# Kernel optimization log

Hardware: AMD Instinct MI355X
Metric: run time of the kernel (lower is better)

The kernel has to match this reference:

```python
import jax, jax.numpy as jnp
import numpy as np

B, S, I, H, O, E, K = 2, 2048, 4096, 1376, 4096, 8, 2
BALANCE_W = 0.01  # balance_loss_weight in llama-moe


def setup_inputs() -> dict:
    key = jax.random.key(0)
    ks = jax.random.split(key, 6)
    sc = lambda k, shape, fan: jax.random.normal(k, shape, jnp.float32) * (fan ** -0.5)
    return {
        "x": jax.random.normal(ks[0], (B, S, I), jnp.float32),
        "gate_w": sc(ks[1], (E, I), I),          # linear gate network, no bias
        "w_gate": sc(ks[2], (E, H, I), I),       # GLU gate proj per expert
        "b_gate": jnp.zeros((E, H), jnp.float32),
        "w_up": sc(ks[3], (E, H, I), I),         # GLU up proj per expert
        "b_up": jnp.zeros((E, H), jnp.float32),
        "w_down": sc(ks[4], (E, O, H), H),       # down proj per expert
        "b_down": jnp.zeros((E, O), jnp.float32),
    }


def _cv_squared(v, eps=1e-10):
    # torch: x.var() / (x.mean()**2 + eps), unbiased variance
    mean = jnp.mean(v)
    var = jnp.sum((v - mean) ** 2) / (v.shape[0] - 1)
    return var / (mean ** 2 + eps)


def reference(x, gate_w, w_gate, b_gate, w_up, b_up, w_down, b_down):
    bsz, seq, _ = x.shape
    xt = x.reshape(-1, I)                         # [T, I] tokens
    T = xt.shape[0]

    # ---- TopKBalancedNoisyGate (no-noise branch) ----
    logits = xt @ gate_w.T                        # [T, E]
    top_logits, top_idx = jax.lax.top_k(logits, K)
    top_scores = jax.nn.softmax(top_logits, axis=-1)   # softmax over top-k logits
    # dense routing matrix: zeros.scatter(1, top_idx, top_scores)
    dense = jnp.zeros((T, E), xt.dtype).at[jnp.arange(T)[:, None], top_idx].set(top_scores)
    importance = dense.sum(axis=0)                # [E]
    load = (dense > 0).astype(jnp.float32).sum(axis=0)  # [E]
    gate_loss = BALANCE_W * (_cv_squared(importance) + _cv_squared(load))

    # ---- UniversalCalculator over LinearGLUExperts ----
    # Dense-dispatch formulation: compute every expert on every token, weight by
    # the (mostly-zero) routing matrix -> identical math to gather/grouped-GEMM/scatter.
    g = jnp.einsum('ti,ehi->teh', xt, w_gate) + b_gate        # [T, E, H]
    u = jnp.einsum('ti,ehi->teh', xt, w_up) + b_up            # [T, E, H]
    inter = jax.nn.silu(g) * u                                # GLU
    # score * (W_down h + b_down) == W_down (score*h) + score*b_down
    y = jnp.einsum('teh,eoh->to', inter * dense[:, :, None], w_down) + dense @ b_down
    return y.reshape(bsz, seq, O), gate_loss
```

## Files before the change

### kernel.cpp

```cpp
#include <hip/hip_runtime.h>
#include <hip/hip_bf16.h>
#include <stdint.h>

#define TN 4096
#define DI 4096
#define DH 1376
#define DHP 1408
#define DO 4096
#define NE 8
#define NPAIR 8192

typedef unsigned short u16;
typedef __bf16 bf16x8 __attribute__((ext_vector_type(8)));
typedef float f32x4 __attribute__((ext_vector_type(4)));
typedef uint32_t u32x4 __attribute__((ext_vector_type(4)));

__device__ __forceinline__ uint32_t pack2bf(float a, float b) {
    union { float f; uint32_t u; } ua, ub;
    ua.f = a; ub.f = b;
    uint32_t lo = (ua.u + 0x7fffu + ((ua.u >> 16) & 1u)) >> 16;
    uint32_t hi = (ub.u + 0x7fffu + ((ub.u >> 16) & 1u)) >> 16;
    return lo | (hi << 16);
}
__device__ __forceinline__ u16 f2bf(float a) {
    union { float f; uint32_t u; } ua; ua.f = a;
    return (u16)((ua.u + 0x7fffu + ((ua.u >> 16) & 1u)) >> 16);
}
__device__ __forceinline__ void gload16(const void* g, void* l) {
    __builtin_amdgcn_global_load_lds(
        (const __attribute__((address_space(1))) void*)g,
        (__attribute__((address_space(3))) void*)l, 16, 0, 0);
}
#define MEMFENCE() asm volatile("" ::: "memory")

__global__ __launch_bounds__(256) void k_cvt_gate(
    const float* __restrict__ x, const float* __restrict__ gw,
    const float* __restrict__ wg, const float* __restrict__ wu,
    const float* __restrict__ wd, const float* __restrict__ bd,
    u16* __restrict__ x16, u16* __restrict__ wg16, u16* __restrict__ wu16,
    u16* __restrict__ wd16,
    int* __restrict__ tke, float* __restrict__ tks,
    int* __restrict__ cnt, float* __restrict__ imp)
{
    int tid = threadIdx.x;
    if (blockIdx.x < TN) {
        int t = blockIdx.x;
        const float* xr = x + (size_t)t * DI;
        double acc[NE];
#pragma unroll
        for (int e = 0; e < NE; ++e) acc[e] = 0.0;
#pragma unroll
        for (int j = 0; j < 4; ++j) {
            int i4 = (j * 256 + tid) * 4;
            float4 xv = *(const float4*)(xr + i4);
            uint2 p; p.x = pack2bf(xv.x, xv.y); p.y = pack2bf(xv.z, xv.w);
            *(uint2*)(x16 + (size_t)t * DI + i4) = p;
#pragma unroll
            for (int e = 0; e < NE; ++e) {
                float4 wv = *(const float4*)(gw + (size_t)e * DI + i4);
                acc[e] = fma((double)xv.x, (double)wv.x, acc[e]);
                acc[e] = fma((double)xv.y, (double)wv.y, acc[e]);
                acc[e] = fma((double)xv.z, (double)wv.z, acc[e]);
                acc[e] = fma((double)xv.w, (double)wv.w, acc[e]);
            }
        }
#pragma unroll
        for (int o = 32; o > 0; o >>= 1)
#pragma unroll
            for (int e = 0; e < NE; ++e) acc[e] += __shfl_down(acc[e], o, 64);
        __shared__ double lred[4][NE];
        if ((tid & 63) == 0)
#pragma unroll
            for (int e = 0; e < NE; ++e) lred[tid >> 6][e] = acc[e];
        __syncthreads();
        if (tid == 0) {
            double lg[NE];
#pragma unroll
            for (int e = 0; e < NE; ++e) lg[e] = lred[0][e] + lred[1][e] + lred[2][e] + lred[3][e];
            int e1 = 0;
            for (int e = 1; e < NE; ++e) if (lg[e] > lg[e1]) e1 = e;
            int e2 = -1;
            for (int e = 0; e < NE; ++e) { if (e == e1) continue; if (e2 < 0 || lg[e] > lg[e2]) e2 = e; }
            float d = (float)(lg[e2] - lg[e1]);
            float ed = expf(d);
            float s1 = 1.0f / (1.0f + ed);
            float s2 = ed / (1.0f + ed);
            tke[2 * t] = e1; tke[2 * t + 1] = e2;
            tks[2 * t] = s1; tks[2 * t + 1] = s2;
            atomicAdd(&cnt[e1], 1); atomicAdd(&cnt[e2], 1);
            unsafeAtomicAdd(&imp[e1], s1); unsafeAtomicAdd(&imp[e2], s2);
        }
        return;
    }
    int i = (blockIdx.x - TN) * 256 + tid;
    if (i < 11272192) {
        const float* src = (i < 5636096) ? wg : wu;
        u16* dst = (i < 5636096) ? wg16 : wu16;
        int j = (i < 5636096) ? i : i - 5636096;
        const float4* s = (const float4*)(src + (size_t)j * 8);
        float4 a = s[0], b = s[1];
        u32x4 v = {pack2bf(a.x, a.y), pack2bf(a.z, a.w), pack2bf(b.x, b.y), pack2bf(b.z, b.w)};
        *(u32x4*)(dst + (size_t)j * 8) = v;
    } else {
        int j = i - 11272192;
        if (j >= 5767168) return;
        int row = j / 176, c8 = (j % 176) * 8;
        u32x4 v = {0u, 0u, 0u, 0u};
        if (c8 < DH) {
            const float4* s = (const float4*)(wd + (size_t)row * DH + c8);
            float4 a = s[0], b = s[1];
            v = (u32x4){pack2bf(a.x, a.y), pack2bf(a.z, a.w), pack2bf(b.x, b.y), pack2bf(b.z, b.w)};
        } else if (c8 == DH) {
            v.x = (uint32_t)f2bf(bd[row]);
        }
        *(u32x4*)(wd16 + (size_t)row * DHP + c8) = v;
    }
}

__global__ __launch_bounds__(256) void k_scatter_fin(
    const int* __restrict__ tke, const float* __restrict__ tks,
    const int* __restrict__ cnt, const float* __restrict__ imp,
    int* __restrict__ off, int* __restrict__ fill,
    int* __restrict__ tok, float* __restrict__ sc, float* __restrict__ loss_out)
{
    int loc[NE]; int o = 0;
#pragma unroll
    for (int e = 0; e < NE; ++e) { loc[e] = o; o += cnt[e]; }
    if (blockIdx.x == 0 && threadIdx.x == 0) {
#pragma unroll
        for (int e = 0; e < NE; ++e) off[e] = loc[e];
        float m1 = 0.f, m2 = 0.f;
        for (int e = 0; e < NE; ++e) { m1 += imp[e]; m2 += (float)cnt[e]; }
        m1 *= 0.125f; m2 *= 0.125f;
        float v1 = 0.f, v2 = 0.f;
        for (int e = 0; e < NE; ++e) {
            float d1 = imp[e] - m1, d2 = (float)cnt[e] - m2;
            v1 += d1 * d1; v2 += d2 * d2;
        }
        v1 /= 7.0f; v2 /= 7.0f;
        *loss_out = 0.01f * (v1 / (m1 * m1 + 1e-10f) + v2 / (m2 * m2 + 1e-10f));
    }
    int t = blockIdx.x * 256 + threadIdx.x;
    if (t >= TN) return;
#pragma unroll
    for (int k = 0; k < 2; ++k) {
        int e = tke[2 * t + k];
        int pos = loc[e] + atomicAdd(&fill[e], 1);
        tok[pos] = t; sc[pos] = tks[2 * t + k];
    }
}

__global__ __launch_bounds__(256, 2) void k_stage1g(
    const u16* __restrict__ x16,
    const u16* __restrict__ wg16, const u16* __restrict__ wu16,
    const float* __restrict__ bg, const float* __restrict__ bu,
    const int* __restrict__ cnt, const int* __restrict__ off,
    const int* __restrict__ tok, const float* __restrict__ sc,
    u16* __restrict__ inter)
{
    int e = blockIdx.x & 7;
    int ce = cnt[e];
    int rows0 = (blockIdx.x >> 3) * 128;
    if (rows0 >= ce) return;
    int oe = off[e];
    int h0 = blockIdx.y * 128;
    int tid = threadIdx.x;

    __shared__ u16 As0[128 * 32]; __shared__ u16 As1[128 * 32]; __shared__ u16 As2[128 * 32];
    __shared__ u16 Gs0[128 * 32]; __shared__ u16 Gs1[128 * 32]; __shared__ u16 Gs2[128 * 32];
    __shared__ u16 Us0[128 * 32]; __shared__ u16 Us1[128 * 32]; __shared__ u16 Us2[128 * 32];

    int swz = ((tid & 3) ^ ((tid >> 3) & 3)) * 8;
    const u16* ab0; const u16* ab1; const u16* gb0; const u16* gb1;
    const u16* ub0; const u16* ub1;
    {
        int rl0 = tid >> 2, rl1 = 64 + (tid >> 2);
        int rg0 = oe + min(rows0 + rl0, ce - 1);
        int rg1 = oe + min(rows0 + rl1, ce - 1);
        ab0 = x16 + (size_t)tok[rg0] * DI + swz;
        ab1 = x16 + (size_t)tok[rg1] * DI + swz;
        int hr0 = min(h0 + rl0, DH - 1), hr1 = min(h0 + rl1, DH - 1);
        gb0 = wg16 + ((size_t)e * DH + hr0) * DI + swz;
        gb1 = wg16 + ((size_t)e * DH + hr1) * DI + swz;
        ub0 = wu16 + ((size_t)e * DH + hr0) * DI + swz;
        ub1 = wu16 + ((size_t)e * DH + hr1) * DI + swz;
    }

    int wid = tid >> 6, lane = tid & 63;
    int ldsw = wid * 512;
    int wm = wid >> 1, wn = wid & 1;
    int rA = wm * 64 + (lane & 15);
    int rB = wn * 64 + (lane & 15);
    int colb = (((lane >> 4) ^ ((lane >> 1) & 3)) & 3) * 8;

    f32x4 accg[4][4], accu[4][4];
    f32x4 vz = {0.f, 0.f, 0.f, 0.f};
#pragma unroll
    for (int m = 0; m < 4; ++m)
#pragma unroll
        for (int n = 0; n < 4; ++n) { accg[m][n] = vz; accu[m][n] = vz; }

#define S1_STAGE(A_, G_, U_, K0)                                   \
    do {                                                           \
        gload16(ab0 + (K0), &A_[ldsw]);                            \
        gload16(ab1 + (K0), &A_[2048 + ldsw]);                     \
        gload16(gb0 + (K0), &G_[ldsw]);                            \
        gload16(gb1 + (K0), &G_[2048 + ldsw]);                     \
        gload16(ub0 + (K0), &U_[ldsw]);                            \
        gload16(ub1 + (K0), &U_[2048 + ldsw]);                     \
    } while (0)

#define S1_COMPUTE(A_, G_, U_)                                     \
    do {                                                           \
        bf16x8 a[4], g[4], u[4];                                   \
        _Pragma("unroll")                                          \
        for (int m = 0; m < 4; ++m)                                \
            a[m] = *(const bf16x8*)&A_[(rA + m * 16) * 32 + colb]; \
        _Pragma("unroll")                                          \
        for (int n = 0; n < 4; ++n) {                              \
            g[n] = *(const bf16x8*)&G_[(rB + n * 16) * 32 + colb]; \
            u[n] = *(const bf16x8*)&U_[(rB + n * 16) * 32 + colb]; \
        }                                                          \
        __builtin_amdgcn_s_setprio(1);                             \
        _Pragma("unroll")                                          \
        for (int m = 0; m < 4; ++m)                                \
            _Pragma("unroll")                                      \
            for (int n = 0; n < 4; ++n) {                          \
                accg[m][n] = __builtin_amdgcn_mfma_f32_16x16x32_bf16(a[m], g[n], accg[m][n], 0, 0, 0); \
                accu[m][n] = __builtin_amdgcn_mfma_f32_16x16x32_bf16(a[m], u[n], accu[m][n], 0, 0, 0); \
            }                                                      \
        __builtin_amdgcn_s_setprio(0);                             \
    } while (0)

#define S1_PHASE(A_, G_, U_, KN)                                   \
    do {                                                           \
        asm volatile("s_waitcnt vmcnt(12)" ::: "memory");          \
        __builtin_amdgcn_s_barrier();                              \
        MEMFENCE();                                                \
        S1_COMPUTE(A_, G_, U_);                                    \
        __builtin_amdgcn_s_barrier();                              \
        MEMFENCE();                                                \
        S1_STAGE(A_, G_, U_, KN);                                  \
    } while (0)

    const int NT = DI / 32;
    const int KL = (NT - 1) * 32;
    S1_STAGE(As0, Gs0, Us0, 0);
    S1_STAGE(As1, Gs1, Us1, 32);
    S1_STAGE(As2, Gs2, Us2, 64);

    for (int kt = 0; kt + 4 < NT; kt += 3) {
        S1_PHASE(As0, Gs0, Us0, min((kt + 3) * 32, KL));
        S1_PHASE(As1, Gs1, Us1, min((kt + 4) * 32, KL));
        S1_PHASE(As2, Gs2, Us2, min((kt + 5) * 32, KL));
    }
    asm volatile("s_waitcnt vmcnt(12)" ::: "memory");
    __builtin_amdgcn_s_barrier();
    MEMFENCE();
    S1_COMPUTE(As0, Gs0, Us0);
    asm volatile("s_waitcnt vmcnt(6)" ::: "memory");
    __builtin_amdgcn_s_barrier();
    MEMFENCE();
    S1_COMPUTE(As1, Gs1, Us1);
    asm volatile("s_waitcnt vmcnt(0)" ::: "memory");
#undef S1_STAGE
#undef S1_COMPUTE
#undef S1_PHASE

    int rmax = ce - rows0;
    float bgv[4], buv[4];
    int hc[4]; bool hok[4];
#pragma unroll
    for (int n = 0; n < 4; ++n) {
        hc[n] = h0 + wn * 64 + n * 16 + (lane & 15);
        hok[n] = hc[n] < DH;
        bgv[n] = hok[n] ? bg[e * DH + hc[n]] : 0.f;
        buv[n] = hok[n] ? bu[e * DH + hc[n]] : 0.f;
    }
#pragma unroll
    for (int m = 0; m < 4; ++m) {
#pragma unroll
        for (int r = 0; r < 4; ++r) {
            int rl = wm * 64 + m * 16 + (lane >> 4) * 4 + r;
            if (rl < rmax) {
                int rg = oe + rows0 + rl;
                float s = sc[rg];
                size_t rowb = (size_t)rg * DHP;
#pragma unroll
                for (int n = 0; n < 4; ++n) {
                    float v = 0.f;
                    if (hok[n]) {
                        float gv = accg[m][n][r] + bgv[n];
                        float uv = accu[m][n][r] + buv[n];
                        float sig = 1.0f / (1.0f + __expf(-gv));
                        v = s * gv * sig * uv;
                    } else if (hc[n] == DH) {
                        v = s;
                    }
                    inter[rowb + hc[n]] = f2bf(v);
                }
            }
        }
    }
}

__global__ __launch_bounds__(256, 2) void k_stage2h(
    const u16* __restrict__ inter, const u16* __restrict__ wd16,
    const int* __restrict__ cnt, const int* __restrict__ off,
    const int* __restrict__ tok, float* __restrict__ y)
{
    int e = blockIdx.x & 7;
    int ce = cnt[e];
    int rows0 = (blockIdx.x >> 3) * 128;
    if (rows0 >= ce) return;
    int oe = off[e];
    int o0 = blockIdx.y * 128;
    int tid = threadIdx.x;

    __shared__ u16 As0[128 * 32]; __shared__ u16 As1[128 * 32];
    __shared__ u16 Bs0[128 * 32]; __shared__ u16 Bs1[128 * 32];

    int swz = ((tid & 3) ^ ((tid >> 3) & 3)) * 8;
    const u16* ab0; const u16* ab1; const u16* bb0; const u16* bb1;
    {
        int rl0 = tid >> 2, rl1 = 64 + (tid >> 2);
        int ar0 = min(oe + rows0 + rl0, NPAIR - 1);
        int ar1 = min(oe + rows0 + rl1, NPAIR - 1);
        ab0 = inter + (size_t)ar0 * DHP + swz;
        ab1 = inter + (size_t)ar1 * DHP + swz;
        bb0 = wd16 + ((size_t)e * DO + (o0 + rl0)) * DHP + swz;
        bb1 = wd16 + ((size_t)e * DO + (o0 + rl1)) * DHP + swz;
    }

    int wid = tid >> 6, lane = tid & 63;
    int ldsw = wid * 512;
    int wm = wid >> 1, wn = wid & 1;
    int rA = wm * 64 + (lane & 15);
    int rB = wn * 64 + (lane & 15);
    int colb = (((lane >> 4) ^ ((lane >> 1) & 3)) & 3) * 8;

    f32x4 acc[4][4];
    f32x4 vz = {0.f, 0.f, 0.f, 0.f};
#pragma unroll
    for (int m = 0; m < 4; ++m)
#pragma unroll
        for (int n = 0; n < 4; ++n) acc[m][n] = vz;

#define S2_STAGE(A_, B_, K0)                                       \
    do {                                                           \
        gload16(ab0 + (K0), &A_[ldsw]);                            \
        gload16(ab1 + (K0), &A_[2048 + ldsw]);                     \
        gload16(bb0 + (K0), &B_[ldsw]);                            \
        gload16(bb1 + (K0), &B_[2048 + ldsw]);                     \
    } while (0)

#define S2_COMPUTE(A_, B_)                                         \
    do {                                                           \
        bf16x8 a[4], b[4];                                         \
        _Pragma("unroll")                                          \
        for (int m = 0; m < 4; ++m)                                \
            a[m] = *(const bf16x8*)&A_[(rA + m * 16) * 32 + colb]; \
        _Pragma("unroll")                                          \
        for (int n = 0; n < 4; ++n)                                \
            b[n] = *(const bf16x8*)&B_[(rB + n * 16) * 32 + colb]; \
        __builtin_amdgcn_s_setprio(1);                             \
        _Pragma("unroll")                                          \
        for (int m = 0; m < 4; ++m)                                \
            _Pragma("unroll")                                      \
            for (int n = 0; n < 4; ++n)                            \
                acc[m][n] = __builtin_amdgcn_mfma_f32_16x16x32_bf16(a[m], b[n], acc[m][n], 0, 0, 0); \
        __builtin_amdgcn_s_setprio(0);                             \
    } while (0)

    const int NT = DHP / 32;
    S2_STAGE(As0, Bs0, 0);
    S2_STAGE(As1, Bs1, 32);

    for (int kt = 0; kt < NT - 2; kt += 2) {
        asm volatile("s_waitcnt vmcnt(4)" ::: "memory");
        __builtin_amdgcn_s_barrier();
        MEMFENCE();
        S2_COMPUTE(As0, Bs0);
        __builtin_amdgcn_s_barrier();
        MEMFENCE();
        S2_STAGE(As0, Bs0, (kt + 2) * 32);
        asm volatile("s_waitcnt vmcnt(4)" ::: "memory");
        __builtin_amdgcn_s_barrier();
        MEMFENCE();
        S2_COMPUTE(As1, Bs1);
        __builtin_amdgcn_s_barrier();
        MEMFENCE();
        S2_STAGE(As1, Bs1, (kt + 3) * 32);
    }
    asm volatile("s_waitcnt vmcnt(4)" ::: "memory");
    __builtin_amdgcn_s_barrier();
    MEMFENCE();
    S2_COMPUTE(As0, Bs0);
    asm volatile("s_waitcnt vmcnt(0)" ::: "memory");
    __builtin_amdgcn_s_barrier();
    MEMFENCE();
    S2_COMPUTE(As1, Bs1);
#undef S2_STAGE
#undef S2_COMPUTE

    int rmax = ce - rows0;
#pragma unroll
    for (int m = 0; m < 4; ++m) {
#pragma unroll
        for (int r = 0; r < 4; ++r) {
            int rl = wm * 64 + m * 16 + (lane >> 4) * 4 + r;
            if (rl >= rmax) continue;
            int t = tok[oe + rows0 + rl];
            float* yr = y + (size_t)t * DO + o0 + wn * 64 + (lane & 15);
#pragma unroll
            for (int n = 0; n < 4; ++n)
                unsafeAtomicAdd(yr + n * 16, acc[m][n][r]);
        }
    }
}

extern "C" void kernel_launch(void* const* d_in, const int* in_sizes, int n_in,
                              void* d_out, int out_size, void* d_ws, size_t ws_size,
                              hipStream_t stream)
{
    const float* x  = (const float*)d_in[0];
    const float* gw = (const float*)d_in[1];
    const float* wg = (const float*)d_in[2];
    const float* bg = (const float*)d_in[3];
    const float* wu = (const float*)d_in[4];
    const float* bu = (const float*)d_in[5];
    const float* wd = (const float*)d_in[6];
    const float* bd = (const float*)d_in[7];
    float* y = (float*)d_out;
    float* loss = y + (size_t)TN * DO;

    uint8_t* ws = (uint8_t*)d_ws;
    u16*   x16   = (u16*)(ws + 0);
    u16*   inter = (u16*)(ws + 33554432ull);
    u16*   wg16  = (u16*)(ws + 56623104ull);
    u16*   wu16  = (u16*)(ws + 146800640ull);
    u16*   wd16  = (u16*)(ws + 236978176ull);
    int*   tok   = (int*)(ws + 329252864ull);
    float* sc    = (float*)(ws + 329285632ull);
    int*   tke   = (int*)(ws + 329318400ull);
    float* tks   = (float*)(ws + 329351168ull);
    int*   misc  = (int*)(ws + 329383936ull);
    int* cnt = misc; int* fill = misc + 8; int* off = misc + 16;
    float* imp = (float*)(misc + 24);

    hipMemsetAsync(misc, 0, 128, stream);
    hipMemsetAsync(d_out, 0, (size_t)out_size * 4, stream);
    k_cvt_gate<<<70656, 256, 0, stream>>>(x, gw, wg, wu, wd, bd,
                                          x16, wg16, wu16, wd16,
                                          tke, tks, cnt, imp);
    k_scatter_fin<<<16, 256, 0, stream>>>(tke, tks, cnt, imp, off, fill, tok, sc, loss);
    k_stage1g<<<dim3(256, 11), 256, 0, stream>>>(x16, wg16, wu16, bg, bu, cnt, off, tok, sc, inter);
    k_stage2h<<<dim3(256, 32), 256, 0, stream>>>(inter, wd16, cnt, off, tok, y);
}
```

Before: 787.2 us.

## Shrink expert GEMM tiles to 128x64 with two-wave blocks for more parallelism

Both grouped GEMM kernels drop from 256-thread 128x128 blocks to 128-thread 128x64 blocks (two waves, each covering 64 rows by all 64 columns). The grid doubles along the H/O dimension, and stage 1 moves from triple to double buffering with smaller LDS use. The goal is more blocks and higher occupancy for load-imbalanced experts. The cost is more re-reads of the gathered activation tiles and more atomics per output.

Measured after the change: 865.7 us. 1.1x slower.

```diff
diff --git a/kernel.cpp b/kernel.cpp
--- a/kernel.cpp
+++ b/kernel.cpp
@@ -150,7 +150,8 @@
     }
 }
 
-__global__ __launch_bounds__(256, 2) void k_stage1g(
+
+__global__ __launch_bounds__(128, 2) void k_stage1s(
     const u16* __restrict__ x16,
     const u16* __restrict__ wg16, const u16* __restrict__ wu16,
     const float* __restrict__ bg, const float* __restrict__ bu,
@@ -163,35 +164,36 @@
     int rows0 = (blockIdx.x >> 3) * 128;
     if (rows0 >= ce) return;
     int oe = off[e];
-    int h0 = blockIdx.y * 128;
+    int h0 = blockIdx.y * 64;
     int tid = threadIdx.x;
 
-    __shared__ u16 As0[128 * 32]; __shared__ u16 As1[128 * 32]; __shared__ u16 As2[128 * 32];
-    __shared__ u16 Gs0[128 * 32]; __shared__ u16 Gs1[128 * 32]; __shared__ u16 Gs2[128 * 32];
-    __shared__ u16 Us0[128 * 32]; __shared__ u16 Us1[128 * 32]; __shared__ u16 Us2[128 * 32];
-
-    int swz = ((tid & 3) ^ ((tid >> 3) & 3)) * 8;
-    const u16* ab0; const u16* ab1; const u16* gb0; const u16* gb1;
-    const u16* ub0; const u16* ub1;
-    {
-        int rl0 = tid >> 2, rl1 = 64 + (tid >> 2);
-        int rg0 = oe + min(rows0 + rl0, ce - 1);
-        int rg1 = oe + min(rows0 + rl1, ce - 1);
-        ab0 = x16 + (size_t)tok[rg0] * DI + swz;
-        ab1 = x16 + (size_t)tok[rg1] * DI + swz;
-        int hr0 = min(h0 + rl0, DH - 1), hr1 = min(h0 + rl1, DH - 1);
-        gb0 = wg16 + ((size_t)e * DH + hr0) * DI + swz;
-        gb1 = wg16 + ((size_t)e * DH + hr1) * DI + swz;
-        ub0 = wu16 + ((size_t)e * DH + hr0) * DI + swz;
-        ub1 = wu16 + ((size_t)e * DH + hr1) * DI + swz;
-    }
-
-    int wid = tid >> 6, lane = tid & 63;
-    int ldsw = wid * 512;
-    int wm = wid >> 1, wn = wid & 1;
-    int rA = wm * 64 + (lane & 15);
-    int rB = wn * 64 + (lane & 15);
+    __shared__ u16 As0[128 * 32]; __shared__ u16 As1[128 * 32];
+    __shared__ u16 Gs0[64 * 32];  __shared__ u16 Gs1[64 * 32];
+    __shared__ u16 Us0[64 * 32];  __shared__ u16 Us1[64 * 32];
+
+    int lane = tid & 63, wid2 = tid >> 6;
+    int swz = ((lane & 3) ^ ((lane >> 3) & 3)) * 8;
+
+    const u16* ab[4];
+#pragma unroll
+    for (int j = 0; j < 4; ++j) {
+        int rowA = j * 32 + wid2 * 16 + (lane >> 2);
+        int rg = oe + min(rows0 + rowA, ce - 1);
+        ab[j] = x16 + (size_t)tok[rg] * DI + swz;
+    }
+    const u16* gb[2]; const u16* ub[2];
+#pragma unroll
+    for (int c = 0; c < 2; ++c) {
+        int rowG = (2 * wid2 + c) * 16 + (lane >> 2);
+        int hr = min(h0 + rowG, DH - 1);
+        gb[c] = wg16 + ((size_t)e * DH + hr) * DI + swz;
+        ub[c] = wu16 + ((size_t)e * DH + hr) * DI + swz;
+    }
+
+    int l15 = lane & 15;
     int colb = (((lane >> 4) ^ ((lane >> 1) & 3)) & 3) * 8;
+    int rA = wid2 * 64 + l15;
+    int rB = l15;
 
     f32x4 accg[4][4], accu[4][4];
     f32x4 vz = {0.f, 0.f, 0.f, 0.f};
@@ -200,79 +202,77 @@
 #pragma unroll
         for (int n = 0; n < 4; ++n) { accg[m][n] = vz; accu[m][n] = vz; }
 
-#define S1_STAGE(A_, G_, U_, K0)                                   \
-    do {                                                           \
-        gload16(ab0 + (K0), &A_[ldsw]);                            \
-        gload16(ab1 + (K0), &A_[2048 + ldsw]);                     \
-        gload16(gb0 + (K0), &G_[ldsw]);                            \
-        gload16(gb1 + (K0), &G_[2048 + ldsw]);                     \
-        gload16(ub0 + (K0), &U_[ldsw]);                            \
-        gload16(ub1 + (K0), &U_[2048 + ldsw]);                     \
+#define S1_STAGE(A_, G_, U_, K0)                                     \
+    do {                                                             \
+        _Pragma("unroll")                                            \
+        for (int j = 0; j < 4; ++j)                                  \
+            gload16(ab[j] + (K0), &A_[j * 1024 + wid2 * 512]);       \
+        _Pragma("unroll")                                            \
+        for (int c = 0; c < 2; ++c) {                                \
+            gload16(gb[c] + (K0), &G_[(2 * wid2 + c) * 512]);        \
+            gload16(ub[c] + (K0), &U_[(2 * wid2 + c) * 512]);        \
+        }                                                            \
     } while (0)
 
-#define S1_COMPUTE(A_, G_, U_)                                     \
-    do {                                                           \
-        bf16x8 a[4], g[4], u[4];                                   \
-        _Pragma("unroll")                                          \
-        for (int m = 0; m < 4; ++m)                                \
-            a[m] = *(const bf16x8*)&A_[(rA + m * 16) * 32 + colb]; \
-        _Pragma("unroll")                                          \
-        for (int n = 0; n < 4; ++n) {                              \
-            g[n] = *(const bf16x8*)&G_[(rB + n * 16) * 32 + colb]; \
-            u[n] = *(const bf16x8*)&U_[(rB + n * 16) * 32 + colb]; \
-        }                                                          \
-        __builtin_amdgcn_s_setprio(1);                             \
-        _Pragma("unroll")                                          \
-        for (int m = 0; m < 4; ++m)                                \
-            _Pragma("unroll")                                      \
-            for (int n = 0; n < 4; ++n) {                          \
+#define S1_COMPUTE(A_, G_, U_)                                       \
+    do {                                                             \
+        bf16x8 a[4], g[4], u[4];                                     \
+        _Pragma("unroll")                                            \
+        for (int m = 0; m < 4; ++m)                                  \
+            a[m] = *(const bf16x8*)&A_[(rA + m * 16) * 32 + colb];   \
+        _Pragma("unroll")                                            \
+        for (int n = 0; n < 4; ++n) {                                \
+            g[n] = *(const bf16x8*)&G_[(rB + n * 16) * 32 + colb];   \
+            u[n] = *(const bf16x8*)&U_[(rB + n * 16) * 32 + colb];   \
+        }                                                            \
+        __builtin_amdgcn_s_setprio(1);                               \
+        _Pragma("unroll")                                            \
+        for (int m = 0; m < 4; ++m)                                  \
+            _Pragma("unroll")                                        \
+            for (int n = 0; n < 4; ++n) {                            \
                 accg[m][n] = __builtin_amdgcn_mfma_f32_16x16x32_bf16(a[m], g[n], accg[m][n], 0, 0, 0); \
                 accu[m][n] = __builtin_amdgcn_mfma_f32_16x16x32_bf16(a[m], u[n], accu[m][n], 0, 0, 0); \
-            }                                                      \
-        __builtin_amdgcn_s_setprio(0);                             \
+            }                                                        \
+        __builtin_amdgcn_s_setprio(0);                               \
     } while (0)
 
-#define S1_PHASE(A_, G_, U_, KN)                                   \
-    do {                                                           \
-        asm volatile("s_waitcnt vmcnt(12)" ::: "memory");          \
-        __builtin_amdgcn_s_barrier();                              \
-        MEMFENCE();                                                \
-        S1_COMPUTE(A_, G_, U_);                                    \
-        __builtin_amdgcn_s_barrier();                              \
-        MEMFENCE();                                                \
-        S1_STAGE(A_, G_, U_, KN);                                  \
-    } while (0)
-
     const int NT = DI / 32;
-    const int KL = (NT - 1) * 32;
     S1_STAGE(As0, Gs0, Us0, 0);
     S1_STAGE(As1, Gs1, Us1, 32);
-    S1_STAGE(As2, Gs2, Us2, 64);
-
-    for (int kt = 0; kt + 4 < NT; kt += 3) {
-        S1_PHASE(As0, Gs0, Us0, min((kt + 3) * 32, KL));
-        S1_PHASE(As1, Gs1, Us1, min((kt + 4) * 32, KL));
-        S1_PHASE(As2, Gs2, Us2, min((kt + 5) * 32, KL));
-    }
-    asm volatile("s_waitcnt vmcnt(12)" ::: "memory");
+
+    for (int kt = 0; kt < NT - 2; kt += 2) {
+        asm volatile("s_waitcnt vmcnt(8)" ::: "memory");
+        __builtin_amdgcn_s_barrier();
+        MEMFENCE();
+        S1_COMPUTE(As0, Gs0, Us0);
+        __builtin_amdgcn_s_barrier();
+        MEMFENCE();
+        S1_STAGE(As0, Gs0, Us0, (kt + 2) * 32);
+        asm volatile("s_waitcnt vmcnt(8)" ::: "memory");
+        __builtin_amdgcn_s_barrier();
+        MEMFENCE();
+        S1_COMPUTE(As1, Gs1, Us1);
+        __builtin_amdgcn_s_barrier();
+        MEMFENCE();
+        S1_STAGE(As1, Gs1, Us1, (kt + 3) * 32);
+    }
+    asm volatile("s_waitcnt vmcnt(8)" ::: "memory");
     __builtin_amdgcn_s_barrier();
     MEMFENCE();
     S1_COMPUTE(As0, Gs0, Us0);
-    asm volatile("s_waitcnt vmcnt(6)" ::: "memory");
+    asm volatile("s_waitcnt vmcnt(0)" ::: "memory");
     __builtin_amdgcn_s_barrier();
     MEMFENCE();
     S1_COMPUTE(As1, Gs1, Us1);
-    asm volatile("s_waitcnt vmcnt(0)" ::: "memory");
 #undef S1_STAGE
 #undef S1_COMPUTE
-#undef S1_PHASE
 
     int rmax = ce - rows0;
     float bgv[4], buv[4];
     int hc[4]; bool hok[4];
 #pragma unroll
     for (int n = 0; n < 4; ++n) {
-        hc[n] = h0 + wn * 64 + n * 16 + (lane & 15);
+        hc[n] = h0 + n * 16 + l15;
         hok[n] = hc[n] < DH;
         bgv[n] = hok[n] ? bg[e * DH + hc[n]] : 0.f;
         buv[n] = hok[n] ? bu[e * DH + hc[n]] : 0.f;
@@ -281,7 +281,7 @@
     for (int m = 0; m < 4; ++m) {
 #pragma unroll
         for (int r = 0; r < 4; ++r) {
-            int rl = wm * 64 + m * 16 + (lane >> 4) * 4 + r;
+            int rl = wid2 * 64 + m * 16 + (lane >> 4) * 4 + r;
             if (rl < rmax) {
                 int rg = oe + rows0 + rl;
                 float s = sc[rg];
@@ -304,7 +304,7 @@
     }
 }
 
-__global__ __launch_bounds__(256, 2) void k_stage2h(
+__global__ __launch_bounds__(128, 3) void k_stage2s(
     const u16* __restrict__ inter, const u16* __restrict__ wd16,
     const int* __restrict__ cnt, const int* __restrict__ off,
     const int* __restrict__ tok, float* __restrict__ y)
@@ -314,30 +314,33 @@
     int rows0 = (blockIdx.x >> 3) * 128;
     if (rows0 >= ce) return;
     int oe = off[e];
-    int o0 = blockIdx.y * 128;
+    int o0 = blockIdx.y * 64;
     int tid = threadIdx.x;
 
     __shared__ u16 As0[128 * 32]; __shared__ u16 As1[128 * 32];
-    __shared__ u16 Bs0[128 * 32]; __shared__ u16 Bs1[128 * 32];
-
-    int swz = ((tid & 3) ^ ((tid >> 3) & 3)) * 8;
-    const u16* ab0; const u16* ab1; const u16* bb0; const u16* bb1;
-    {
-        int rl0 = tid >> 2, rl1 = 64 + (tid >> 2);
-        int ar0 = min(oe + rows0 + rl0, NPAIR - 1);
-        int ar1 = min(oe + rows0 + rl1, NPAIR - 1);
-        ab0 = inter + (size_t)ar0 * DHP + swz;
-        ab1 = inter + (size_t)ar1 * DHP + swz;
-        bb0 = wd16 + ((size_t)e * DO + (o0 + rl0)) * DHP + swz;
-        bb1 = wd16 + ((size_t)e * DO + (o0 + rl1)) * DHP + swz;
-    }
-
-    int wid = tid >> 6, lane = tid & 63;
-    int ldsw = wid * 512;
-    int wm = wid >> 1, wn = wid & 1;
-    int rA = wm * 64 + (lane & 15);
-    int rB = wn * 64 + (lane & 15);
+    __shared__ u16 Bs0[64 * 32];  __shared__ u16 Bs1[64 * 32];
+
+    int lane = tid & 63, wid2 = tid >> 6;
+    int swz = ((lane & 3) ^ ((lane >> 3) & 3)) * 8;
+
+    const u16* ab[4];
+#pragma unroll
+    for (int j = 0; j < 4; ++j) {
+        int rowA = j * 32 + wid2 * 16 + (lane >> 2);
+        int ar = min(oe + rows0 + rowA, NPAIR - 1);
+        ab[j] = inter + (size_t)ar * DHP + swz;
+    }
+    const u16* bb[2];
+#pragma unroll
+    for (int c = 0; c < 2; ++c) {
+        int rowB = (2 * wid2 + c) * 16 + (lane >> 2);
+        bb[c] = wd16 + ((size_t)e * DO + (o0 + rowB)) * DHP + swz;
+    }
+
+    int l15 = lane & 15;
     int colb = (((lane >> 4) ^ ((lane >> 1) & 3)) & 3) * 8;
+    int rA = wid2 * 64 + l15;
+    int rB = l15;
 
     f32x4 acc[4][4];
     f32x4 vz = {0.f, 0.f, 0.f, 0.f};
@@ -346,30 +349,32 @@
 #pragma unroll
         for (int n = 0; n < 4; ++n) acc[m][n] = vz;
 
-#define S2_STAGE(A_, B_, K0)                                       \
-    do {                                                           \
-        gload16(ab0 + (K0), &A_[ldsw]);                            \
-        gload16(ab1 + (K0), &A_[2048 + ldsw]);                     \
-        gload16(bb0 + (K0), &B_[ldsw]);                            \
-        gload16(bb1 + (K0), &B_[2048 + ldsw]);                     \
+#define S2_STAGE(A_, B_, K0)                                         \
+    do {                                                             \
+        _Pragma("unroll")                                            \
+        for (int j = 0; j < 4; ++j)                                  \
+            gload16(ab[j] + (K0), &A_[j * 1024 + wid2 * 512]);       \
+        _Pragma("unroll")                                            \
+        for (int c = 0; c < 2; ++c)                                  \
+            gload16(bb[c] + (K0), &B_[(2 * wid2 + c) * 512]);        \
     } while (0)
 
-#define S2_COMPUTE(A_, B_)                                         \
-    do {                                                           \
-        bf16x8 a[4], b[4];                                         \
-        _Pragma("unroll")                                          \
-        for (int m = 0; m < 4; ++m)                                \
-            a[m] = *(const bf16x8*)&A_[(rA + m * 16) * 32 + colb]; \
-        _Pragma("unroll")                                          \
-        for (int n = 0; n < 4; ++n)                                \
-            b[n] = *(const bf16x8*)&B_[(rB + n * 16) * 32 + colb]; \
-        __builtin_amdgcn_s_setprio(1);                             \
-        _Pragma("unroll")                                          \
-        for (int m = 0; m < 4; ++m)                                \
-            _Pragma("unroll")                                      \
-            for (int n = 0; n < 4; ++n)                            \
+#define S2_COMPUTE(A_, B_)                                           \
+    do {                                                             \
+        bf16x8 a[4], b[4];                                           \
+        _Pragma("unroll")                                            \
+        for (int m = 0; m < 4; ++m)                                  \
+            a[m] = *(const bf16x8*)&A_[(rA + m * 16) * 32 + colb];   \
+        _Pragma("unroll")                                            \
+        for (int n = 0; n < 4; ++n)                                  \
+            b[n] = *(const bf16x8*)&B_[(rB + n * 16) * 32 + colb];   \
+        __builtin_amdgcn_s_setprio(1);                               \
+        _Pragma("unroll")                                            \
+        for (int m = 0; m < 4; ++m)                                  \
+            _Pragma("unroll")                                        \
+            for (int n = 0; n < 4; ++n)                              \
                 acc[m][n] = __builtin_amdgcn_mfma_f32_16x16x32_bf16(a[m], b[n], acc[m][n], 0, 0, 0); \
-        __builtin_amdgcn_s_setprio(0);                             \
+        __builtin_amdgcn_s_setprio(0);                               \
     } while (0)
 
     const int NT = DHP / 32;
@@ -377,14 +382,14 @@
     S2_STAGE(As1, Bs1, 32);
 
     for (int kt = 0; kt < NT - 2; kt += 2) {
-        asm volatile("s_waitcnt vmcnt(4)" ::: "memory");
+        asm volatile("s_waitcnt vmcnt(6)" ::: "memory");
         __builtin_amdgcn_s_barrier();
         MEMFENCE();
         S2_COMPUTE(As0, Bs0);
         __builtin_amdgcn_s_barrier();
         MEMFENCE();
         S2_STAGE(As0, Bs0, (kt + 2) * 32);
-        asm volatile("s_waitcnt vmcnt(4)" ::: "memory");
+        asm volatile("s_waitcnt vmcnt(6)" ::: "memory");
         __builtin_amdgcn_s_barrier();
         MEMFENCE();
         S2_COMPUTE(As1, Bs1);
@@ -392,7 +397,7 @@
         MEMFENCE();
         S2_STAGE(As1, Bs1, (kt + 3) * 32);
     }
-    asm volatile("s_waitcnt vmcnt(4)" ::: "memory");
+    asm volatile("s_waitcnt vmcnt(6)" ::: "memory");
     __builtin_amdgcn_s_barrier();
     MEMFENCE();
     S2_COMPUTE(As0, Bs0);
@@ -408,10 +413,10 @@
     for (int m = 0; m < 4; ++m) {
 #pragma unroll
         for (int r = 0; r < 4; ++r) {
-            int rl = wm * 64 + m * 16 + (lane >> 4) * 4 + r;
+            int rl = wid2 * 64 + m * 16 + (lane >> 4) * 4 + r;
             if (rl >= rmax) continue;
             int t = tok[oe + rows0 + rl];
-            float* yr = y + (size_t)t * DO + o0 + wn * 64 + (lane & 15);
+            float* yr = y + (size_t)t * DO + o0 + l15;
 #pragma unroll
             for (int n = 0; n < 4; ++n)
                 unsafeAtomicAdd(yr + n * 16, acc[m][n][r]);
@@ -454,6 +459,6 @@
                                           x16, wg16, wu16, wd16,
                                           tke, tks, cnt, imp);
     k_scatter_fin<<<16, 256, 0, stream>>>(tke, tks, cnt, imp, off, fill, tok, sc, loss);
-    k_stage1g<<<dim3(256, 11), 256, 0, stream>>>(x16, wg16, wu16, bg, bu, cnt, off, tok, sc, inter);
-    k_stage2h<<<dim3(256, 32), 256, 0, stream>>>(inter, wd16, cnt, off, tok, y);
-}
+    k_stage1s<<<dim3(256, 22), 128, 0, stream>>>(x16, wg16, wu16, bg, bu, cnt, off, tok, sc, inter);
+    k_stage2s<<<dim3(256, 64), 128, 0, stream>>>(inter, wd16, cnt, off, tok, y);
+}
```

## Replace atomic scatter-add of expert outputs with bf16 partials plus gather reduce

Applied to the files above, without the earlier changes.

Stage 2 now writes each (token, expert) pair's down-projection result as bf16 into a per-pair buffer that reuses the wg16 workspace, instead of atomically adding fp32 into y. The scatter kernel records each token's two pair positions, and a new reduce kernel sums the two partial rows per token into y, which also removes the memset of the output. This drops the float atomics and the output zeroing, at the cost of an extra kernel, an extra bf16 round-trip of the partial results, and a bf16 rounding step before the sum.

Result: faster. 754.7 us (-4.1%).

```diff
diff --git a/kernel.cpp b/kernel.cpp
--- a/kernel.cpp
+++ b/kernel.cpp
@@ -25,6 +25,12 @@
 __device__ __forceinline__ u16 f2bf(float a) {
     union { float f; uint32_t u; } ua; ua.f = a;
     return (u16)((ua.u + 0x7fffu + ((ua.u >> 16) & 1u)) >> 16);
+}
+__device__ __forceinline__ float bflo(uint32_t u) {
+    union { uint32_t u; float f; } v; v.u = u << 16; return v.f;
+}
+__device__ __forceinline__ float bfhi(uint32_t u) {
+    union { uint32_t u; float f; } v; v.u = u & 0xffff0000u; return v.f;
 }
 __device__ __forceinline__ void gload16(const void* g, void* l) {
     __builtin_amdgcn_global_load_lds(
@@ -118,7 +124,8 @@
 }
 
 __global__ __launch_bounds__(256) void k_scatter_fin(
-    const int* __restrict__ tke, const float* __restrict__ tks,
+    int* __restrict__ tke ,
+    const float* __restrict__ tks,
     const int* __restrict__ cnt, const float* __restrict__ imp,
     int* __restrict__ off, int* __restrict__ fill,
     int* __restrict__ tok, float* __restrict__ sc, float* __restrict__ loss_out)
@@ -142,12 +149,12 @@
     }
     int t = blockIdx.x * 256 + threadIdx.x;
     if (t >= TN) return;
-#pragma unroll
-    for (int k = 0; k < 2; ++k) {
-        int e = tke[2 * t + k];
-        int pos = loc[e] + atomicAdd(&fill[e], 1);
-        tok[pos] = t; sc[pos] = tks[2 * t + k];
-    }
+    int e0 = tke[2 * t], e1 = tke[2 * t + 1];
+    float s0 = tks[2 * t], s1 = tks[2 * t + 1];
+    int p0 = loc[e0] + atomicAdd(&fill[e0], 1);
+    tok[p0] = t; sc[p0] = s0; tke[2 * t] = p0;
+    int p1 = loc[e1] + atomicAdd(&fill[e1], 1);
+    tok[p1] = t; sc[p1] = s1; tke[2 * t + 1] = p1;
 }
 
 __global__ __launch_bounds__(256, 2) void k_stage1g(
@@ -304,10 +311,10 @@
     }
 }
 
-__global__ __launch_bounds__(256, 2) void k_stage2h(
+__global__ __launch_bounds__(256, 2) void k_stage2p(
     const u16* __restrict__ inter, const u16* __restrict__ wd16,
     const int* __restrict__ cnt, const int* __restrict__ off,
-    const int* __restrict__ tok, float* __restrict__ y)
+    u16* __restrict__ ypart)
 {
     int e = blockIdx.x & 7;
     int ce = cnt[e];
@@ -410,12 +417,32 @@
         for (int r = 0; r < 4; ++r) {
             int rl = wm * 64 + m * 16 + (lane >> 4) * 4 + r;
             if (rl >= rmax) continue;
-            int t = tok[oe + rows0 + rl];
-            float* yr = y + (size_t)t * DO + o0 + wn * 64 + (lane & 15);
+            size_t rowb = (size_t)(oe + rows0 + rl) * DO + o0 + wn * 64 + (lane & 15);
 #pragma unroll
             for (int n = 0; n < 4; ++n)
-                unsafeAtomicAdd(yr + n * 16, acc[m][n][r]);
-        }
+                ypart[rowb + n * 16] = f2bf(acc[m][n][r]);
+        }
+    }
+}
+
+__global__ __launch_bounds__(256) void k_reduce(
+    const u16* __restrict__ ypart, const int* __restrict__ tpos,
+    float* __restrict__ y)
+{
+    int t = blockIdx.x, tid = threadIdx.x;
+    int p0 = tpos[2 * t], p1 = tpos[2 * t + 1];
+    int c = tid * 16;
+    const u16* r0 = ypart + (size_t)p0 * DO + c;
+    const u16* r1 = ypart + (size_t)p1 * DO + c;
+    float* yr = y + (size_t)t * DO + c;
+    u32x4 a0 = *(const u32x4*)r0, a1 = *(const u32x4*)(r0 + 8);
+    u32x4 b0 = *(const u32x4*)r1, b1 = *(const u32x4*)(r1 + 8);
+    uint32_t ua[8] = {a0.x, a0.y, a0.z, a0.w, a1.x, a1.y, a1.z, a1.w};
+    uint32_t ub[8] = {b0.x, b0.y, b0.z, b0.w, b1.x, b1.y, b1.z, b1.w};
+#pragma unroll
+    for (int j = 0; j < 8; ++j) {
+        yr[2 * j]     = bflo(ua[j]) + bflo(ub[j]);
+        yr[2 * j + 1] = bfhi(ua[j]) + bfhi(ub[j]);
     }
 }
 
@@ -447,13 +474,14 @@
     int*   misc  = (int*)(ws + 329383936ull);
     int* cnt = misc; int* fill = misc + 8; int* off = misc + 16;
     float* imp = (float*)(misc + 24);
+    u16* ypart = wg16;
 
     hipMemsetAsync(misc, 0, 128, stream);
-    hipMemsetAsync(d_out, 0, (size_t)out_size * 4, stream);
     k_cvt_gate<<<70656, 256, 0, stream>>>(x, gw, wg, wu, wd, bd,
                                           x16, wg16, wu16, wd16,
                                           tke, tks, cnt, imp);
     k_scatter_fin<<<16, 256, 0, stream>>>(tke, tks, cnt, imp, off, fill, tok, sc, loss);
     k_stage1g<<<dim3(256, 11), 256, 0, stream>>>(x16, wg16, wu16, bg, bu, cnt, off, tok, sc, inter);
-    k_stage2h<<<dim3(256, 32), 256, 0, stream>>>(inter, wd16, cnt, off, tok, y);
-}
+    k_stage2p<<<dim3(256, 32), 256, 0, stream>>>(inter, wd16, cnt, off, ypart);
+    k_reduce<<<TN, 256, 0, stream>>>(ypart, tke, y);
+}
```
